# Kernel tuning notes

Measured on AMD Instinct MI355X. Metric: run time of the kernel, lower is better.

Reference implementation:

```python
import jax, jax.numpy as jnp
import numpy as np

NUM_HEADS = 8
QUERY_HEAD_DIM = 32
POS_HEAD_DIM = 4
EMBED_DIM = 512
POS_DIM = 192
SEQ_LEN = 1024
BATCH = 8
IN_PROJ_DIM = (QUERY_HEAD_DIM * 2 + POS_HEAD_DIM) * NUM_HEADS  # 544


def setup_inputs() -> dict:
    key = jax.random.key(0)
    k1, k2, k3, k4, k5 = jax.random.split(key, 5)
    x = jax.random.normal(k1, (SEQ_LEN, BATCH, EMBED_DIM), dtype=jnp.float32)
    pos_emb = jax.random.normal(k2, (1, 2 * SEQ_LEN - 1, POS_DIM), dtype=jnp.float32)
    key_padding_mask = jnp.zeros((BATCH, SEQ_LEN), dtype=bool)
    # in_proj: ScaledLinear(embed_dim -> in_proj_dim) with initial_scale qhd**-0.25
    scale_in = QUERY_HEAD_DIM ** (-0.25) / np.sqrt(EMBED_DIM)
    W_in = jax.random.normal(k3, (EMBED_DIM, IN_PROJ_DIM), dtype=jnp.float32) * scale_in
    b_in = jax.random.normal(k4, (IN_PROJ_DIM,), dtype=jnp.float32) * 0.01
    # linear_pos: ScaledLinear(pos_dim -> num_heads*pos_head_dim), no bias, scale 0.05
    W_pos = jax.random.normal(k5, (POS_DIM, NUM_HEADS * POS_HEAD_DIM), dtype=jnp.float32) * (0.05 / np.sqrt(POS_DIM))
    return {"x": x, "pos_emb": pos_emb, "W_in": W_in, "b_in": b_in,
            "W_pos": W_pos, "key_padding_mask": key_padding_mask}


def reference(x, pos_emb, W_in, b_in, W_pos, key_padding_mask):
    S, B, _ = x.shape
    H, QH, PH = NUM_HEADS, QUERY_HEAD_DIM, POS_HEAD_DIM
    qd = H * QH
    xp = x @ W_in + b_in                          # (S, B, in_proj_dim)
    q = xp[..., :qd].reshape(S, B, H, QH)
    k = xp[..., qd:2 * qd].reshape(S, B, H, QH)   # Whiten/Balancer are identity in eval
    p = xp[..., 2 * qd:].reshape(S, B, H, PH)
    # content scores: (H, B, T, Sk)
    attn_scores = jnp.einsum('tbhd,sbhd->hbts', q, k)
    # positional scores
    pe = (pos_emb @ W_pos).reshape(2 * S - 1, H, PH)          # (2S-1, H, PH)
    pos_scores = jnp.einsum('tbhd,nhd->hbtn', p, pe)          # (H, B, T, 2S-1)
    # relative shift: out[h,b,t,j] = pos_scores[h,b,t, (S-1) - t + j]
    idx = (S - 1) - jnp.arange(S)[:, None] + jnp.arange(S)[None, :]  # (S, S)
    shifted = jnp.take_along_axis(pos_scores, idx[None, None, :, :], axis=-1)
    attn_scores = attn_scores + shifted
    # key padding mask: True positions get -1000 (as in masked_fill)
    attn_scores = jnp.where(key_padding_mask[None, :, None, :], -1000.0, attn_scores)
    return jax.nn.softmax(attn_scores, axis=-1)  # (H, B, T, S)
```

## Files before the change

### kernel.cpp

```cpp
#include <hip/hip_runtime.h>

#define SEQ  1024
#define BATCH 8
#define NH   8
#define EMB  512
#define QHD  32
#define PHD  4
#define PDIM 192
#define NPROJ 544
#define NPE  2047
#define L2E  1.4426950408889634f

typedef float nf4 __attribute__((ext_vector_type(4)));
typedef short bf16x8 __attribute__((ext_vector_type(8)));
typedef float f32x4 __attribute__((ext_vector_type(4)));

__device__ __forceinline__ unsigned short f2bf_rne(float f) {
    unsigned int u = __float_as_uint(f);
    unsigned int r = (u + 0x7fffu + ((u >> 16) & 1u)) >> 16;
    return (unsigned short)r;
}
__device__ __forceinline__ float bf2f(unsigned short b) {
    return __uint_as_float(((unsigned int)b) << 16);
}
__device__ __forceinline__ void cvt8(const float4 a, const float4 b, uint4& hi, uint4& lo) {
    unsigned short h0 = f2bf_rne(a.x), h1 = f2bf_rne(a.y), h2 = f2bf_rne(a.z), h3 = f2bf_rne(a.w);
    unsigned short h4 = f2bf_rne(b.x), h5 = f2bf_rne(b.y), h6 = f2bf_rne(b.z), h7 = f2bf_rne(b.w);
    unsigned short l0 = f2bf_rne(a.x - bf2f(h0)), l1 = f2bf_rne(a.y - bf2f(h1));
    unsigned short l2 = f2bf_rne(a.z - bf2f(h2)), l3 = f2bf_rne(a.w - bf2f(h3));
    unsigned short l4 = f2bf_rne(b.x - bf2f(h4)), l5 = f2bf_rne(b.y - bf2f(h5));
    unsigned short l6 = f2bf_rne(b.z - bf2f(h6)), l7 = f2bf_rne(b.w - bf2f(h7));
    hi.x = (unsigned)h0 | ((unsigned)h1 << 16); hi.y = (unsigned)h2 | ((unsigned)h3 << 16);
    hi.z = (unsigned)h4 | ((unsigned)h5 << 16); hi.w = (unsigned)h6 | ((unsigned)h7 << 16);
    lo.x = (unsigned)l0 | ((unsigned)l1 << 16); lo.y = (unsigned)l2 | ((unsigned)l3 << 16);
    lo.z = (unsigned)l4 | ((unsigned)l5 << 16); lo.w = (unsigned)l6 | ((unsigned)l7 << 16);
}

__global__ __launch_bounds__(256) void convw_kernel(const float* __restrict__ W,
                                                    unsigned short* __restrict__ whT,
                                                    unsigned short* __restrict__ wlT) {
    __shared__ float tile[32][33];
    const int n0 = blockIdx.x * 32, k0 = blockIdx.y * 32;
    const int c = threadIdx.x & 31, r0 = threadIdx.x >> 5;
#pragma unroll
    for (int i = 0; i < 4; ++i) {
        int r = r0 + i * 8;
        tile[r][c] = W[(size_t)(k0 + r) * NPROJ + n0 + c];
    }
    __syncthreads();
#pragma unroll
    for (int i = 0; i < 4; ++i) {
        int n = r0 + i * 8;
        float v = tile[c][n];
        unsigned short h = f2bf_rne(v);
        unsigned short l = f2bf_rne(v - bf2f(h));
        whT[(size_t)(n0 + n) * 512 + k0 + c] = h;
        wlT[(size_t)(n0 + n) * 512 + k0 + c] = l;
    }
}

__global__ __launch_bounds__(128) void pe_kernel(const float* __restrict__ pos_emb,
                                                 const float* __restrict__ W_pos,
                                                 float* __restrict__ peg) {
    const int n = blockIdx.x * 128 + threadIdx.x;
    const int h = blockIdx.y;
    if (n >= NPE) return;
    const float* pr = pos_emb + (size_t)n * PDIM;
    float a0 = 0.f, a1 = 0.f, a2 = 0.f, a3 = 0.f;
    for (int c = 0; c < PDIM; c += 4) {
        float4 pv = *(const float4*)(pr + c);
#pragma unroll
        for (int cc = 0; cc < 4; ++cc) {
            float pvc = cc == 0 ? pv.x : cc == 1 ? pv.y : cc == 2 ? pv.z : pv.w;
            float4 w4 = *(const float4*)(W_pos + (c + cc) * 32 + h * 4);
            a0 += pvc * w4.x; a1 += pvc * w4.y; a2 += pvc * w4.z; a3 += pvc * w4.w;
        }
    }
    float4 o;
    o.x = a0 * L2E; o.y = a1 * L2E; o.z = a2 * L2E; o.w = a3 * L2E;
    *(float4*)(peg + ((size_t)h * NPE + n) * 4) = o;
}

__global__ __launch_bounds__(256) void inproj_kernel(const float* __restrict__ x,
                                                     const unsigned short* __restrict__ whT,
                                                     const unsigned short* __restrict__ wlT,
                                                     const float* __restrict__ bias,
                                                     unsigned short* __restrict__ qhi,
                                                     unsigned short* __restrict__ qlo,
                                                     unsigned short* __restrict__ khi,
                                                     unsigned short* __restrict__ klo,
                                                     float* __restrict__ pws) {
    __shared__ __align__(16) unsigned short xh_l[8][128][8];
    __shared__ __align__(16) unsigned short xl_l[8][128][8];
    __shared__ __align__(16) unsigned short wh_l[8][32][8];
    __shared__ __align__(16) unsigned short wl_l[8][32][8];

    const int tid = threadIdx.x, lane = tid & 63, w = tid >> 6;
    const int la = lane & 15, lb = lane >> 4;
    const int m0 = blockIdx.x * 128, n0 = blockIdx.y * 32;

    const int mx = tid >> 1, k8x = (tid & 1) * 4;
    const int nw = tid >> 3, k8w = tid & 7;

    f32x4 acc[2][2];
#pragma unroll
    for (int mt = 0; mt < 2; ++mt)
#pragma unroll
        for (int nt = 0; nt < 2; ++nt) acc[mt][nt] = (f32x4){0.f, 0.f, 0.f, 0.f};

    for (int step = 0; step < 8; ++step) {
        const int k0 = step * 64;
        const float* sx = x + (size_t)(m0 + mx) * EMB + k0 + k8x * 8;
#pragma unroll
        for (int j = 0; j < 4; ++j) {
            float4 a = *(const float4*)(sx + j * 8);
            float4 b = *(const float4*)(sx + j * 8 + 4);
            uint4 hi, lo;
            cvt8(a, b, hi, lo);
            *(uint4*)&xh_l[k8x + j][mx][0] = hi;
            *(uint4*)&xl_l[k8x + j][mx][0] = lo;
        }
        *(uint4*)&wh_l[k8w][nw][0] = *(const uint4*)(whT + (size_t)(n0 + nw) * 512 + k0 + k8w * 8);
        *(uint4*)&wl_l[k8w][nw][0] = *(const uint4*)(wlT + (size_t)(n0 + nw) * 512 + k0 + k8w * 8);
        __syncthreads();
#pragma unroll
        for (int ks = 0; ks < 2; ++ks) {
            bf16x8 bh[2], bl[2], ah[2], al[2];
#pragma unroll
            for (int mt = 0; mt < 2; ++mt) {
                bh[mt] = *(const bf16x8*)&xh_l[ks * 4 + lb][w * 32 + mt * 16 + la][0];
                bl[mt] = *(const bf16x8*)&xl_l[ks * 4 + lb][w * 32 + mt * 16 + la][0];
            }
#pragma unroll
            for (int nt = 0; nt < 2; ++nt) {
                ah[nt] = *(const bf16x8*)&wh_l[ks * 4 + lb][nt * 16 + la][0];
                al[nt] = *(const bf16x8*)&wl_l[ks * 4 + lb][nt * 16 + la][0];
            }
#pragma unroll
            for (int mt = 0; mt < 2; ++mt)
#pragma unroll
                for (int nt = 0; nt < 2; ++nt) {
                    acc[mt][nt] = __builtin_amdgcn_mfma_f32_16x16x32_bf16(ah[nt], bh[mt], acc[mt][nt], 0, 0, 0);
                    acc[mt][nt] = __builtin_amdgcn_mfma_f32_16x16x32_bf16(ah[nt], bl[mt], acc[mt][nt], 0, 0, 0);
                    acc[mt][nt] = __builtin_amdgcn_mfma_f32_16x16x32_bf16(al[nt], bh[mt], acc[mt][nt], 0, 0, 0);
                }
        }
        __syncthreads();
    }

    const int by = blockIdx.y;
#pragma unroll
    for (int mt = 0; mt < 2; ++mt) {
        const int m = m0 + w * 32 + mt * 16 + la;
        const int s = m >> 3, bb = m & 7;
#pragma unroll
        for (int nt = 0; nt < 2; ++nt) {
            const int dloc = nt * 16 + lb * 4;
            float4 b4 = *(const float4*)(bias + n0 + dloc);
            float v0 = acc[mt][nt][0] + b4.x;
            float v1 = acc[mt][nt][1] + b4.y;
            float v2 = acc[mt][nt][2] + b4.z;
            float v3 = acc[mt][nt][3] + b4.w;
            if (by < 16) {
                const int h = by & 7;
                size_t base = (((size_t)(h * 8 + bb) * SEQ + s) * 32 + dloc);
                if (by < 8) {
                    v0 *= L2E; v1 *= L2E; v2 *= L2E; v3 *= L2E;
                }
                ushort4 hi, lo;
                hi.x = f2bf_rne(v0); lo.x = f2bf_rne(v0 - bf2f(hi.x));
                hi.y = f2bf_rne(v1); lo.y = f2bf_rne(v1 - bf2f(hi.y));
                hi.z = f2bf_rne(v2); lo.z = f2bf_rne(v2 - bf2f(hi.z));
                hi.w = f2bf_rne(v3); lo.w = f2bf_rne(v3 - bf2f(hi.w));
                if (by < 8) {
                    *(ushort4*)(qhi + base) = hi;
                    *(ushort4*)(qlo + base) = lo;
                } else {
                    *(ushort4*)(khi + base) = hi;
                    *(ushort4*)(klo + base) = lo;
                }
            } else {
                const int h = nt * 4 + lb;
                float4 o; o.x = v0; o.y = v1; o.z = v2; o.w = v3;
                *(float4*)(pws + ((size_t)(h * 8 + bb) * SEQ + s) * 4) = o;
            }
        }
    }
}

__global__ __launch_bounds__(256, 3) void attn_kernel(const unsigned short* __restrict__ qhi,
                                                      const unsigned short* __restrict__ qlo,
                                                      const unsigned short* __restrict__ khi,
                                                      const unsigned short* __restrict__ klo,
                                                      const float* __restrict__ pws,
                                                      const float* __restrict__ peg,
                                                      const unsigned char* __restrict__ km,
                                                      float* __restrict__ out) {
    __shared__ float4 pe_lds[1040];
    __shared__ float red_s[16][4];

    const int bid = blockIdx.x;
    const int hb = bid & 63;
    const int h = hb >> 3, b = hb & 7;
    const int t0 = (bid >> 6) * 16;
    const int tid = threadIdx.x, lane = tid & 63;
    const int j_s = tid >> 6;
    const int la = lane & 15, lb = lane >> 4;

    const int nbase = (SEQ - 1) - t0 - 15;
    const float4* pegq = (const float4*)peg + (size_t)h * NPE + nbase;
#pragma unroll
    for (int it = 0; it < 5; ++it) {
        int idx = it * 256 + tid;
        if (idx < 1039) pe_lds[idx] = pegq[idx];
    }
    __syncthreads();

    const int t = t0 + la;
    const size_t qoff = ((size_t)hb * SEQ + t) * 32 + lb * 8;
    const bf16x8 bqh = *(const bf16x8*)(qhi + qoff);
    const bf16x8 bql = *(const bf16x8*)(qlo + qoff);

    const unsigned short* khb = khi + (size_t)hb * (SEQ * 32);
    const unsigned short* klb = klo + (size_t)hb * (SEQ * 32);

    f32x4 acc[16];
#pragma unroll
    for (int m = 0; m < 16; ++m) acc[m] = (f32x4){0.f, 0.f, 0.f, 0.f};

#pragma unroll
    for (int m = 0; m < 16; ++m) {
        const int srow = j_s * 256 + m * 16 + la;
        const bf16x8 ah = *(const bf16x8*)(khb + (size_t)srow * 32 + lb * 8);
        const bf16x8 al = *(const bf16x8*)(klb + (size_t)srow * 32 + lb * 8);
        acc[m] = __builtin_amdgcn_mfma_f32_16x16x32_bf16(ah, bqh, acc[m], 0, 0, 0);
        acc[m] = __builtin_amdgcn_mfma_f32_16x16x32_bf16(ah, bql, acc[m], 0, 0, 0);
        acc[m] = __builtin_amdgcn_mfma_f32_16x16x32_bf16(al, bqh, acc[m], 0, 0, 0);
    }

    const float4 pvv = *(const float4*)(pws + ((size_t)hb * SEQ + t) * 4);
    const int lane_off = j_s * 256 + lb * 4 + 15 - la;
#pragma unroll
    for (int m = 0; m < 16; ++m) {
        const int o = lane_off + m * 16;
#pragma unroll
        for (int j = 0; j < 4; ++j) {
            float4 e = pe_lds[o + j];
            acc[m][j] += pvv.x * e.x + pvv.y * e.y + pvv.z * e.z + pvv.w * e.w;
        }
    }

    const unsigned int* kmw = (const unsigned int*)(km + b * SEQ);
    unsigned int mk[16], mor = 0;
#pragma unroll
    for (int m = 0; m < 16; ++m) { mk[m] = kmw[j_s * 64 + m * 4 + lb]; mor |= mk[m]; }
    if (__any(mor != 0)) {
#pragma unroll
        for (int m = 0; m < 16; ++m) {
            if (mk[m] & 0x000000ffu) acc[m][0] = -1443.0f;
            if (mk[m] & 0x0000ff00u) acc[m][1] = -1443.0f;
            if (mk[m] & 0x00ff0000u) acc[m][2] = -1443.0f;
            if (mk[m] & 0xff000000u) acc[m][3] = -1443.0f;
        }
    }

    float sum = 0.f;
#pragma unroll
    for (int m = 0; m < 16; ++m) {
        acc[m][0] = __builtin_amdgcn_exp2f(acc[m][0]);
        acc[m][1] = __builtin_amdgcn_exp2f(acc[m][1]);
        acc[m][2] = __builtin_amdgcn_exp2f(acc[m][2]);
        acc[m][3] = __builtin_amdgcn_exp2f(acc[m][3]);
        sum += (acc[m][0] + acc[m][1]) + (acc[m][2] + acc[m][3]);
    }
    sum += __shfl_xor(sum, 16, 64);
    sum += __shfl_xor(sum, 32, 64);
    if (lane < 16) red_s[lane][j_s] = sum;
    __syncthreads();
    const float inv = 1.0f / ((red_s[la][0] + red_s[la][1]) + (red_s[la][2] + red_s[la][3]));

    float* op = out + ((size_t)hb * SEQ + t) * SEQ;
#pragma unroll
    for (int m = 0; m < 16; ++m) {
        nf4 o;
        o.x = acc[m][0] * inv;
        o.y = acc[m][1] * inv;
        o.z = acc[m][2] * inv;
        o.w = acc[m][3] * inv;
        __builtin_nontemporal_store(o, (nf4*)(op + j_s * 256 + m * 16 + lb * 4));
    }
}

extern "C" void kernel_launch(void* const* d_in, const int* in_sizes, int n_in,
                              void* d_out, int out_size, void* d_ws, size_t ws_size,
                              hipStream_t stream) {
    const float* x       = (const float*)d_in[0];
    const float* pos_emb = (const float*)d_in[1];
    const float* W_in    = (const float*)d_in[2];
    const float* b_in    = (const float*)d_in[3];
    const float* W_pos   = (const float*)d_in[4];
    const unsigned char* km = (const unsigned char*)d_in[5];
    float* out = (float*)d_out;

    char* ws = (char*)d_ws;
    const size_t MB = 1024 * 1024;
    unsigned short* qhi = (unsigned short*)(ws);
    unsigned short* qlo = (unsigned short*)(ws + 4 * MB);
    unsigned short* khi = (unsigned short*)(ws + 8 * MB);
    unsigned short* klo = (unsigned short*)(ws + 12 * MB);
    float*          pws = (float*)(ws + 16 * MB);
    float*          peg = (float*)(ws + 17 * MB);
    unsigned short* whT = (unsigned short*)(ws + 18 * MB);
    unsigned short* wlT = (unsigned short*)(ws + 19 * MB);

    hipLaunchKernelGGL(convw_kernel, dim3(17, 16), dim3(256), 0, stream, W_in, whT, wlT);
    hipLaunchKernelGGL(pe_kernel, dim3(16, 8), dim3(128), 0, stream, pos_emb, W_pos, peg);
    hipLaunchKernelGGL(inproj_kernel, dim3(64, 17), dim3(256), 0, stream,
                       x, whT, wlT, b_in, qhi, qlo, khi, klo, pws);
    hipLaunchKernelGGL(attn_kernel, dim3(4096), dim3(256), 0, stream,
                       qhi, qlo, khi, klo, pws, peg, km, out);
}
```

Measured before the change: 154.5 us.

## Pre-split x to bf16 hi/lo, interleave K hi/lo, widen attention blocks

Adds a separate kernel that converts x to bf16 hi/lo once, instead of each inproj block reconverting it (x is reread 17 times across the N tiles). K hi and lo are stored interleaved per 8-element group so each attention lane fetches hi and lo from adjacent memory. The attention kernel moves to 512 threads with 8 waves, each handling 128 keys with half the accumulators, which lowers register pressure and changes the occupancy target. The cost is an extra kernel launch and a write plus reread of the 16 MB hi/lo copy of x.

```diff
diff --git a/kernel.cpp b/kernel.cpp
--- a/kernel.cpp
+++ b/kernel.cpp
@@ -23,17 +23,24 @@
 __device__ __forceinline__ float bf2f(unsigned short b) {
     return __uint_as_float(((unsigned int)b) << 16);
 }
-__device__ __forceinline__ void cvt8(const float4 a, const float4 b, uint4& hi, uint4& lo) {
-    unsigned short h0 = f2bf_rne(a.x), h1 = f2bf_rne(a.y), h2 = f2bf_rne(a.z), h3 = f2bf_rne(a.w);
-    unsigned short h4 = f2bf_rne(b.x), h5 = f2bf_rne(b.y), h6 = f2bf_rne(b.z), h7 = f2bf_rne(b.w);
-    unsigned short l0 = f2bf_rne(a.x - bf2f(h0)), l1 = f2bf_rne(a.y - bf2f(h1));
-    unsigned short l2 = f2bf_rne(a.z - bf2f(h2)), l3 = f2bf_rne(a.w - bf2f(h3));
-    unsigned short l4 = f2bf_rne(b.x - bf2f(h4)), l5 = f2bf_rne(b.y - bf2f(h5));
-    unsigned short l6 = f2bf_rne(b.z - bf2f(h6)), l7 = f2bf_rne(b.w - bf2f(h7));
-    hi.x = (unsigned)h0 | ((unsigned)h1 << 16); hi.y = (unsigned)h2 | ((unsigned)h3 << 16);
-    hi.z = (unsigned)h4 | ((unsigned)h5 << 16); hi.w = (unsigned)h6 | ((unsigned)h7 << 16);
-    lo.x = (unsigned)l0 | ((unsigned)l1 << 16); lo.y = (unsigned)l2 | ((unsigned)l3 << 16);
-    lo.z = (unsigned)l4 | ((unsigned)l5 << 16); lo.w = (unsigned)l6 | ((unsigned)l7 << 16);
+
+__global__ __launch_bounds__(256) void convx_kernel(const float* __restrict__ x,
+                                                    unsigned short* __restrict__ xhi,
+                                                    unsigned short* __restrict__ xlo) {
+    int i = (blockIdx.x * 256 + threadIdx.x) * 8;
+    float4 a = *(const float4*)(x + i);
+    float4 b = *(const float4*)(x + i + 4);
+    ushort4 h0, l0, h1, l1;
+    h0.x = f2bf_rne(a.x); l0.x = f2bf_rne(a.x - bf2f(h0.x));
+    h0.y = f2bf_rne(a.y); l0.y = f2bf_rne(a.y - bf2f(h0.y));
+    h0.z = f2bf_rne(a.z); l0.z = f2bf_rne(a.z - bf2f(h0.z));
+    h0.w = f2bf_rne(a.w); l0.w = f2bf_rne(a.w - bf2f(h0.w));
+    h1.x = f2bf_rne(b.x); l1.x = f2bf_rne(b.x - bf2f(h1.x));
+    h1.y = f2bf_rne(b.y); l1.y = f2bf_rne(b.y - bf2f(h1.y));
+    h1.z = f2bf_rne(b.z); l1.z = f2bf_rne(b.z - bf2f(h1.z));
+    h1.w = f2bf_rne(b.w); l1.w = f2bf_rne(b.w - bf2f(h1.w));
+    *(ushort4*)(xhi + i) = h0; *(ushort4*)(xhi + i + 4) = h1;
+    *(ushort4*)(xlo + i) = l0; *(ushort4*)(xlo + i + 4) = l1;
 }
 
 __global__ __launch_bounds__(256) void convw_kernel(const float* __restrict__ W,
@@ -81,14 +88,14 @@
     *(float4*)(peg + ((size_t)h * NPE + n) * 4) = o;
 }
 
-__global__ __launch_bounds__(256) void inproj_kernel(const float* __restrict__ x,
+__global__ __launch_bounds__(256) void inproj_kernel(const unsigned short* __restrict__ xhi,
+                                                     const unsigned short* __restrict__ xlo,
                                                      const unsigned short* __restrict__ whT,
                                                      const unsigned short* __restrict__ wlT,
                                                      const float* __restrict__ bias,
                                                      unsigned short* __restrict__ qhi,
                                                      unsigned short* __restrict__ qlo,
-                                                     unsigned short* __restrict__ khi,
-                                                     unsigned short* __restrict__ klo,
+                                                     unsigned short* __restrict__ kint,
                                                      float* __restrict__ pws) {
     __shared__ __align__(16) unsigned short xh_l[8][128][8];
     __shared__ __align__(16) unsigned short xl_l[8][128][8];
@@ -110,15 +117,12 @@
 
     for (int step = 0; step < 8; ++step) {
         const int k0 = step * 64;
-        const float* sx = x + (size_t)(m0 + mx) * EMB + k0 + k8x * 8;
+        const unsigned short* sxh = xhi + (size_t)(m0 + mx) * 512 + k0 + k8x * 8;
+        const unsigned short* sxl = xlo + (size_t)(m0 + mx) * 512 + k0 + k8x * 8;
 #pragma unroll
         for (int j = 0; j < 4; ++j) {
-            float4 a = *(const float4*)(sx + j * 8);
-            float4 b = *(const float4*)(sx + j * 8 + 4);
-            uint4 hi, lo;
-            cvt8(a, b, hi, lo);
-            *(uint4*)&xh_l[k8x + j][mx][0] = hi;
-            *(uint4*)&xl_l[k8x + j][mx][0] = lo;
+            *(uint4*)&xh_l[k8x + j][mx][0] = *(const uint4*)(sxh + j * 8);
+            *(uint4*)&xl_l[k8x + j][mx][0] = *(const uint4*)(sxl + j * 8);
         }
         *(uint4*)&wh_l[k8w][nw][0] = *(const uint4*)(whT + (size_t)(n0 + nw) * 512 + k0 + k8w * 8);
         *(uint4*)&wl_l[k8w][nw][0] = *(const uint4*)(wlT + (size_t)(n0 + nw) * 512 + k0 + k8w * 8);
@@ -161,24 +165,28 @@
             float v1 = acc[mt][nt][1] + b4.y;
             float v2 = acc[mt][nt][2] + b4.z;
             float v3 = acc[mt][nt][3] + b4.w;
-            if (by < 16) {
-                const int h = by & 7;
+            if (by < 8) {
+                const int h = by;
                 size_t base = (((size_t)(h * 8 + bb) * SEQ + s) * 32 + dloc);
-                if (by < 8) {
-                    v0 *= L2E; v1 *= L2E; v2 *= L2E; v3 *= L2E;
-                }
+                v0 *= L2E; v1 *= L2E; v2 *= L2E; v3 *= L2E;
                 ushort4 hi, lo;
                 hi.x = f2bf_rne(v0); lo.x = f2bf_rne(v0 - bf2f(hi.x));
                 hi.y = f2bf_rne(v1); lo.y = f2bf_rne(v1 - bf2f(hi.y));
                 hi.z = f2bf_rne(v2); lo.z = f2bf_rne(v2 - bf2f(hi.z));
                 hi.w = f2bf_rne(v3); lo.w = f2bf_rne(v3 - bf2f(hi.w));
-                if (by < 8) {
-                    *(ushort4*)(qhi + base) = hi;
-                    *(ushort4*)(qlo + base) = lo;
-                } else {
-                    *(ushort4*)(khi + base) = hi;
-                    *(ushort4*)(klo + base) = lo;
-                }
+                *(ushort4*)(qhi + base) = hi;
+                *(ushort4*)(qlo + base) = lo;
+            } else if (by < 16) {
+                const int h = by - 8;
+                const int grp = dloc >> 3, off8 = dloc & 7;
+                size_t base = (((size_t)(h * 8 + bb) * SEQ + s) * 4 + grp) * 16 + off8;
+                ushort4 hi, lo;
+                hi.x = f2bf_rne(v0); lo.x = f2bf_rne(v0 - bf2f(hi.x));
+                hi.y = f2bf_rne(v1); lo.y = f2bf_rne(v1 - bf2f(hi.y));
+                hi.z = f2bf_rne(v2); lo.z = f2bf_rne(v2 - bf2f(hi.z));
+                hi.w = f2bf_rne(v3); lo.w = f2bf_rne(v3 - bf2f(hi.w));
+                *(ushort4*)(kint + base) = hi;
+                *(ushort4*)(kint + base + 8) = lo;
             } else {
                 const int h = nt * 4 + lb;
                 float4 o; o.x = v0; o.y = v1; o.z = v2; o.w = v3;
@@ -188,30 +196,28 @@
     }
 }
 
-__global__ __launch_bounds__(256, 3) void attn_kernel(const unsigned short* __restrict__ qhi,
+__global__ __launch_bounds__(512, 2) void attn_kernel(const unsigned short* __restrict__ qhi,
                                                       const unsigned short* __restrict__ qlo,
-                                                      const unsigned short* __restrict__ khi,
-                                                      const unsigned short* __restrict__ klo,
+                                                      const unsigned short* __restrict__ kint,
                                                       const float* __restrict__ pws,
                                                       const float* __restrict__ peg,
                                                       const unsigned char* __restrict__ km,
                                                       float* __restrict__ out) {
     __shared__ float4 pe_lds[1040];
-    __shared__ float red_s[16][4];
+    __shared__ float red_s[16][8];
 
     const int bid = blockIdx.x;
     const int hb = bid & 63;
     const int h = hb >> 3, b = hb & 7;
     const int t0 = (bid >> 6) * 16;
-    const int tid = threadIdx.x, lane = tid & 63;
-    const int j_s = tid >> 6;
+    const int tid = threadIdx.x, lane = tid & 63, w = tid >> 6;
     const int la = lane & 15, lb = lane >> 4;
 
     const int nbase = (SEQ - 1) - t0 - 15;
     const float4* pegq = (const float4*)peg + (size_t)h * NPE + nbase;
 #pragma unroll
-    for (int it = 0; it < 5; ++it) {
-        int idx = it * 256 + tid;
+    for (int it = 0; it < 3; ++it) {
+        int idx = it * 512 + tid;
         if (idx < 1039) pe_lds[idx] = pegq[idx];
     }
     __syncthreads();
@@ -221,27 +227,27 @@
     const bf16x8 bqh = *(const bf16x8*)(qhi + qoff);
     const bf16x8 bql = *(const bf16x8*)(qlo + qoff);
 
-    const unsigned short* khb = khi + (size_t)hb * (SEQ * 32);
-    const unsigned short* klb = klo + (size_t)hb * (SEQ * 32);
-
-    f32x4 acc[16];
-#pragma unroll
-    for (int m = 0; m < 16; ++m) acc[m] = (f32x4){0.f, 0.f, 0.f, 0.f};
-
-#pragma unroll
-    for (int m = 0; m < 16; ++m) {
-        const int srow = j_s * 256 + m * 16 + la;
-        const bf16x8 ah = *(const bf16x8*)(khb + (size_t)srow * 32 + lb * 8);
-        const bf16x8 al = *(const bf16x8*)(klb + (size_t)srow * 32 + lb * 8);
+    const unsigned short* kb = kint + (size_t)hb * (SEQ * 64);
+
+    f32x4 acc[8];
+#pragma unroll
+    for (int m = 0; m < 8; ++m) acc[m] = (f32x4){0.f, 0.f, 0.f, 0.f};
+
+#pragma unroll
+    for (int m = 0; m < 8; ++m) {
+        const int srow = w * 128 + m * 16 + la;
+        const unsigned short* p = kb + ((size_t)srow * 4 + lb) * 16;
+        const bf16x8 ah = *(const bf16x8*)p;
+        const bf16x8 al = *(const bf16x8*)(p + 8);
         acc[m] = __builtin_amdgcn_mfma_f32_16x16x32_bf16(ah, bqh, acc[m], 0, 0, 0);
         acc[m] = __builtin_amdgcn_mfma_f32_16x16x32_bf16(ah, bql, acc[m], 0, 0, 0);
         acc[m] = __builtin_amdgcn_mfma_f32_16x16x32_bf16(al, bqh, acc[m], 0, 0, 0);
     }
 
     const float4 pvv = *(const float4*)(pws + ((size_t)hb * SEQ + t) * 4);
-    const int lane_off = j_s * 256 + lb * 4 + 15 - la;
-#pragma unroll
-    for (int m = 0; m < 16; ++m) {
+    const int lane_off = w * 128 + lb * 4 + 15 - la;
+#pragma unroll
+    for (int m = 0; m < 8; ++m) {
         const int o = lane_off + m * 16;
 #pragma unroll
         for (int j = 0; j < 4; ++j) {
@@ -251,12 +257,12 @@
     }
 
     const unsigned int* kmw = (const unsigned int*)(km + b * SEQ);
-    unsigned int mk[16], mor = 0;
-#pragma unroll
-    for (int m = 0; m < 16; ++m) { mk[m] = kmw[j_s * 64 + m * 4 + lb]; mor |= mk[m]; }
+    unsigned int mk[8], mor = 0;
+#pragma unroll
+    for (int m = 0; m < 8; ++m) { mk[m] = kmw[w * 32 + m * 4 + lb]; mor |= mk[m]; }
     if (__any(mor != 0)) {
 #pragma unroll
-        for (int m = 0; m < 16; ++m) {
+        for (int m = 0; m < 8; ++m) {
             if (mk[m] & 0x000000ffu) acc[m][0] = -1443.0f;
             if (mk[m] & 0x0000ff00u) acc[m][1] = -1443.0f;
             if (mk[m] & 0x00ff0000u) acc[m][2] = -1443.0f;
@@ -266,7 +272,7 @@
 
     float sum = 0.f;
 #pragma unroll
-    for (int m = 0; m < 16; ++m) {
+    for (int m = 0; m < 8; ++m) {
         acc[m][0] = __builtin_amdgcn_exp2f(acc[m][0]);
         acc[m][1] = __builtin_amdgcn_exp2f(acc[m][1]);
         acc[m][2] = __builtin_amdgcn_exp2f(acc[m][2]);
@@ -275,19 +281,20 @@
     }
     sum += __shfl_xor(sum, 16, 64);
     sum += __shfl_xor(sum, 32, 64);
-    if (lane < 16) red_s[lane][j_s] = sum;
+    if (lane < 16) red_s[lane][w] = sum;
     __syncthreads();
-    const float inv = 1.0f / ((red_s[la][0] + red_s[la][1]) + (red_s[la][2] + red_s[la][3]));
+    const float inv = 1.0f / (((red_s[la][0] + red_s[la][1]) + (red_s[la][2] + red_s[la][3])) +
+                              ((red_s[la][4] + red_s[la][5]) + (red_s[la][6] + red_s[la][7])));
 
     float* op = out + ((size_t)hb * SEQ + t) * SEQ;
 #pragma unroll
-    for (int m = 0; m < 16; ++m) {
+    for (int m = 0; m < 8; ++m) {
         nf4 o;
         o.x = acc[m][0] * inv;
         o.y = acc[m][1] * inv;
         o.z = acc[m][2] * inv;
         o.w = acc[m][3] * inv;
-        __builtin_nontemporal_store(o, (nf4*)(op + j_s * 256 + m * 16 + lb * 4));
+        __builtin_nontemporal_store(o, (nf4*)(op + w * 128 + m * 16 + lb * 4));
     }
 }
 
@@ -304,19 +311,21 @@
 
     char* ws = (char*)d_ws;
     const size_t MB = 1024 * 1024;
-    unsigned short* qhi = (unsigned short*)(ws);
-    unsigned short* qlo = (unsigned short*)(ws + 4 * MB);
-    unsigned short* khi = (unsigned short*)(ws + 8 * MB);
-    unsigned short* klo = (unsigned short*)(ws + 12 * MB);
-    float*          pws = (float*)(ws + 16 * MB);
-    float*          peg = (float*)(ws + 17 * MB);
-    unsigned short* whT = (unsigned short*)(ws + 18 * MB);
-    unsigned short* wlT = (unsigned short*)(ws + 19 * MB);
-
+    unsigned short* qhi  = (unsigned short*)(ws);
+    unsigned short* qlo  = (unsigned short*)(ws + 4 * MB);
+    unsigned short* kint = (unsigned short*)(ws + 8 * MB);
+    float*          pws  = (float*)(ws + 16 * MB);
+    float*          peg  = (float*)(ws + 17 * MB);
+    unsigned short* xhi  = (unsigned short*)(ws + 18 * MB);
+    unsigned short* xlo  = (unsigned short*)(ws + 26 * MB);
+    unsigned short* whT  = (unsigned short*)(ws + 34 * MB);
+    unsigned short* wlT  = (unsigned short*)(ws + 35 * MB);
+
+    hipLaunchKernelGGL(convx_kernel, dim3(2048), dim3(256), 0, stream, x, xhi, xlo);
     hipLaunchKernelGGL(convw_kernel, dim3(17, 16), dim3(256), 0, stream, W_in, whT, wlT);
     hipLaunchKernelGGL(pe_kernel, dim3(16, 8), dim3(128), 0, stream, pos_emb, W_pos, peg);
     hipLaunchKernelGGL(inproj_kernel, dim3(64, 17), dim3(256), 0, stream,
-                       x, whT, wlT, b_in, qhi, qlo, khi, klo, pws);
-    hipLaunchKernelGGL(attn_kernel, dim3(4096), dim3(256), 0, stream,
-                       qhi, qlo, khi, klo, pws, peg, km, out);
-}
+                       xhi, xlo, whT, wlT, b_in, qhi, qlo, kint, pws);
+    hipLaunchKernelGGL(attn_kernel, dim3(4096), dim3(512), 0, stream,
+                       qhi, qlo, kint, pws, peg, km, out);
+}
```

Measured after the change: 161.5 us. 4.5% more time.

## Retile in-projection GEMM so each block covers several N-tiles and prefetches x

Applied to the files above, without the earlier changes.

The in-projection kernel now uses 64-row M tiles and has each block compute 4 or 5 of the 17 output column tiles. Each x tile is converted to bf16 hi/lo once and reused across those column tiles, instead of being reconverted for every one of the 17. The next x tile is loaded into registers while the current one is being computed, and outputs are written with nontemporal stores. The grid shrinks from 1088 to 512 blocks, and register and LDS use per block grow, which may lower occupancy.

```diff
diff --git a/kernel.cpp b/kernel.cpp
--- a/kernel.cpp
+++ b/kernel.cpp
@@ -12,6 +12,7 @@
 #define L2E  1.4426950408889634f
 
 typedef float nf4 __attribute__((ext_vector_type(4)));
+typedef unsigned short us4 __attribute__((ext_vector_type(4)));
 typedef short bf16x8 __attribute__((ext_vector_type(8)));
 typedef float f32x4 __attribute__((ext_vector_type(4)));
 
@@ -90,99 +91,119 @@
                                                      unsigned short* __restrict__ khi,
                                                      unsigned short* __restrict__ klo,
                                                      float* __restrict__ pws) {
-    __shared__ __align__(16) unsigned short xh_l[8][128][8];
-    __shared__ __align__(16) unsigned short xl_l[8][128][8];
-    __shared__ __align__(16) unsigned short wh_l[8][32][8];
-    __shared__ __align__(16) unsigned short wl_l[8][32][8];
+    __shared__ __align__(16) unsigned short xh_l[8][64][8];
+    __shared__ __align__(16) unsigned short xl_l[8][64][8];
+    __shared__ __align__(16) unsigned short wh_l[5][8][32][8];
+    __shared__ __align__(16) unsigned short wl_l[5][8][32][8];
+
+    const int mb = blockIdx.x;
+    const int g  = blockIdx.y;
+    const int start = (g == 0) ? 0 : (1 + g * 4);
+    const int G     = (g == 0) ? 5 : 4;
+    const int m0 = mb * 64;
 
     const int tid = threadIdx.x, lane = tid & 63, w = tid >> 6;
     const int la = lane & 15, lb = lane >> 4;
-    const int m0 = blockIdx.x * 128, n0 = blockIdx.y * 32;
-
-    const int mx = tid >> 1, k8x = (tid & 1) * 4;
+
+    const int rx = tid >> 2, kx = (tid & 3) * 16;
     const int nw = tid >> 3, k8w = tid & 7;
 
-    f32x4 acc[2][2];
-#pragma unroll
-    for (int mt = 0; mt < 2; ++mt)
-#pragma unroll
-        for (int nt = 0; nt < 2; ++nt) acc[mt][nt] = (f32x4){0.f, 0.f, 0.f, 0.f};
+    const float* sx = x + (size_t)(m0 + rx) * EMB + kx;
+    float4 xa[4];
+#pragma unroll
+    for (int j = 0; j < 4; ++j) xa[j] = *(const float4*)(sx + j * 4);
+
+    f32x4 acc[5][2];
+#pragma unroll
+    for (int j = 0; j < 5; ++j)
+#pragma unroll
+        for (int nt = 0; nt < 2; ++nt) acc[j][nt] = (f32x4){0.f, 0.f, 0.f, 0.f};
 
     for (int step = 0; step < 8; ++step) {
         const int k0 = step * 64;
-        const float* sx = x + (size_t)(m0 + mx) * EMB + k0 + k8x * 8;
-#pragma unroll
-        for (int j = 0; j < 4; ++j) {
-            float4 a = *(const float4*)(sx + j * 8);
-            float4 b = *(const float4*)(sx + j * 8 + 4);
-            uint4 hi, lo;
-            cvt8(a, b, hi, lo);
-            *(uint4*)&xh_l[k8x + j][mx][0] = hi;
-            *(uint4*)&xl_l[k8x + j][mx][0] = lo;
-        }
-        *(uint4*)&wh_l[k8w][nw][0] = *(const uint4*)(whT + (size_t)(n0 + nw) * 512 + k0 + k8w * 8);
-        *(uint4*)&wl_l[k8w][nw][0] = *(const uint4*)(wlT + (size_t)(n0 + nw) * 512 + k0 + k8w * 8);
+        {
+            uint4 hi0, lo0, hi1, lo1;
+            cvt8(xa[0], xa[1], hi0, lo0);
+            cvt8(xa[2], xa[3], hi1, lo1);
+            const int k8 = (tid & 3) * 2;
+            *(uint4*)&xh_l[k8][rx][0]     = hi0;
+            *(uint4*)&xl_l[k8][rx][0]     = lo0;
+            *(uint4*)&xh_l[k8 + 1][rx][0] = hi1;
+            *(uint4*)&xl_l[k8 + 1][rx][0] = lo1;
+        }
+#pragma unroll
+        for (int j = 0; j < 5; ++j) {
+            if (j < G) {
+                const size_t wo = (size_t)((start + j) * 32 + nw) * 512 + k0 + k8w * 8;
+                *(uint4*)&wh_l[j][k8w][nw][0] = *(const uint4*)(whT + wo);
+                *(uint4*)&wl_l[j][k8w][nw][0] = *(const uint4*)(wlT + wo);
+            }
+        }
+        if (step < 7) {
+            sx += 64;
+#pragma unroll
+            for (int j = 0; j < 4; ++j) xa[j] = *(const float4*)(sx + j * 4);
+        }
         __syncthreads();
 #pragma unroll
         for (int ks = 0; ks < 2; ++ks) {
-            bf16x8 bh[2], bl[2], ah[2], al[2];
-#pragma unroll
-            for (int mt = 0; mt < 2; ++mt) {
-                bh[mt] = *(const bf16x8*)&xh_l[ks * 4 + lb][w * 32 + mt * 16 + la][0];
-                bl[mt] = *(const bf16x8*)&xl_l[ks * 4 + lb][w * 32 + mt * 16 + la][0];
+            const int k8 = ks * 4 + lb;
+            const bf16x8 bh = *(const bf16x8*)&xh_l[k8][w * 16 + la][0];
+            const bf16x8 bl = *(const bf16x8*)&xl_l[k8][w * 16 + la][0];
+#pragma unroll
+            for (int j = 0; j < 5; ++j) {
+                if (j < G) {
+#pragma unroll
+                    for (int nt = 0; nt < 2; ++nt) {
+                        const bf16x8 ah = *(const bf16x8*)&wh_l[j][k8][nt * 16 + la][0];
+                        const bf16x8 al = *(const bf16x8*)&wl_l[j][k8][nt * 16 + la][0];
+                        acc[j][nt] = __builtin_amdgcn_mfma_f32_16x16x32_bf16(ah, bh, acc[j][nt], 0, 0, 0);
+                        acc[j][nt] = __builtin_amdgcn_mfma_f32_16x16x32_bf16(ah, bl, acc[j][nt], 0, 0, 0);
+                        acc[j][nt] = __builtin_amdgcn_mfma_f32_16x16x32_bf16(al, bh, acc[j][nt], 0, 0, 0);
+                    }
+                }
             }
+        }
+        __syncthreads();
+    }
+
+    const int m = m0 + w * 16 + la;
+    const int s = m >> 3, bb = m & 7;
+#pragma unroll
+    for (int j = 0; j < 5; ++j) {
+        if (j < G) {
+            const int by = start + j;
+            const int n0 = by * 32;
 #pragma unroll
             for (int nt = 0; nt < 2; ++nt) {
-                ah[nt] = *(const bf16x8*)&wh_l[ks * 4 + lb][nt * 16 + la][0];
-                al[nt] = *(const bf16x8*)&wl_l[ks * 4 + lb][nt * 16 + la][0];
-            }
-#pragma unroll
-            for (int mt = 0; mt < 2; ++mt)
-#pragma unroll
-                for (int nt = 0; nt < 2; ++nt) {
-                    acc[mt][nt] = __builtin_amdgcn_mfma_f32_16x16x32_bf16(ah[nt], bh[mt], acc[mt][nt], 0, 0, 0);
-                    acc[mt][nt] = __builtin_amdgcn_mfma_f32_16x16x32_bf16(ah[nt], bl[mt], acc[mt][nt], 0, 0, 0);
-                    acc[mt][nt] = __builtin_amdgcn_mfma_f32_16x16x32_bf16(al[nt], bh[mt], acc[mt][nt], 0, 0, 0);
+                const int dloc = nt * 16 + lb * 4;
+                float4 b4 = *(const float4*)(bias + n0 + dloc);
+                float v0 = acc[j][nt][0] + b4.x;
+                float v1 = acc[j][nt][1] + b4.y;
+                float v2 = acc[j][nt][2] + b4.z;
+                float v3 = acc[j][nt][3] + b4.w;
+                if (by < 16) {
+                    const int h = by & 7;
+                    size_t base = (((size_t)(h * 8 + bb) * SEQ + s) * 32 + dloc);
+                    if (by < 8) { v0 *= L2E; v1 *= L2E; v2 *= L2E; v3 *= L2E; }
+                    us4 hi, lo;
+                    hi.x = f2bf_rne(v0); lo.x = f2bf_rne(v0 - bf2f(hi.x));
+                    hi.y = f2bf_rne(v1); lo.y = f2bf_rne(v1 - bf2f(hi.y));
+                    hi.z = f2bf_rne(v2); lo.z = f2bf_rne(v2 - bf2f(hi.z));
+                    hi.w = f2bf_rne(v3); lo.w = f2bf_rne(v3 - bf2f(hi.w));
+                    if (by < 8) {
+                        __builtin_nontemporal_store(hi, (us4*)(qhi + base));
+                        __builtin_nontemporal_store(lo, (us4*)(qlo + base));
+                    } else {
+                        __builtin_nontemporal_store(hi, (us4*)(khi + base));
+                        __builtin_nontemporal_store(lo, (us4*)(klo + base));
+                    }
+                } else {
+                    const int hh = nt * 4 + lb;
+                    nf4 o;
+                    o.x = v0; o.y = v1; o.z = v2; o.w = v3;
+                    __builtin_nontemporal_store(o, (nf4*)(pws + ((size_t)(hh * 8 + bb) * SEQ + s) * 4));
                 }
-        }
-        __syncthreads();
-    }
-
-    const int by = blockIdx.y;
-#pragma unroll
-    for (int mt = 0; mt < 2; ++mt) {
-        const int m = m0 + w * 32 + mt * 16 + la;
-        const int s = m >> 3, bb = m & 7;
-#pragma unroll
-        for (int nt = 0; nt < 2; ++nt) {
-            const int dloc = nt * 16 + lb * 4;
-            float4 b4 = *(const float4*)(bias + n0 + dloc);
-            float v0 = acc[mt][nt][0] + b4.x;
-            float v1 = acc[mt][nt][1] + b4.y;
-            float v2 = acc[mt][nt][2] + b4.z;
-            float v3 = acc[mt][nt][3] + b4.w;
-            if (by < 16) {
-                const int h = by & 7;
-                size_t base = (((size_t)(h * 8 + bb) * SEQ + s) * 32 + dloc);
-                if (by < 8) {
-                    v0 *= L2E; v1 *= L2E; v2 *= L2E; v3 *= L2E;
-                }
-                ushort4 hi, lo;
-                hi.x = f2bf_rne(v0); lo.x = f2bf_rne(v0 - bf2f(hi.x));
-                hi.y = f2bf_rne(v1); lo.y = f2bf_rne(v1 - bf2f(hi.y));
-                hi.z = f2bf_rne(v2); lo.z = f2bf_rne(v2 - bf2f(hi.z));
-                hi.w = f2bf_rne(v3); lo.w = f2bf_rne(v3 - bf2f(hi.w));
-                if (by < 8) {
-                    *(ushort4*)(qhi + base) = hi;
-                    *(ushort4*)(qlo + base) = lo;
-                } else {
-                    *(ushort4*)(khi + base) = hi;
-                    *(ushort4*)(klo + base) = lo;
-                }
-            } else {
-                const int h = nt * 4 + lb;
-                float4 o; o.x = v0; o.y = v1; o.z = v2; o.w = v3;
-                *(float4*)(pws + ((size_t)(h * 8 + bb) * SEQ + s) * 4) = o;
             }
         }
     }
@@ -315,7 +336,7 @@
 
     hipLaunchKernelGGL(convw_kernel, dim3(17, 16), dim3(256), 0, stream, W_in, whT, wlT);
     hipLaunchKernelGGL(pe_kernel, dim3(16, 8), dim3(128), 0, stream, pos_emb, W_pos, peg);
-    hipLaunchKernelGGL(inproj_kernel, dim3(64, 17), dim3(256), 0, stream,
+    hipLaunchKernelGGL(inproj_kernel, dim3(128, 4), dim3(256), 0, stream,
                        x, whT, wlT, b_in, qhi, qlo, khi, klo, pws);
     hipLaunchKernelGGL(attn_kernel, dim3(4096), dim3(256), 0, stream,
                        qhi, qlo, khi, klo, pws, peg, km, out);
```

Measured after the change: 163.3 us. 5.7% more time.
